# Kernel tuning notes

Hardware: AMD Instinct MI355X
Metric: run time of the kernel (lower is better)

Reference implementation:

```python
import jax, jax.numpy as jnp
import numpy as np

INPUT_DIM = 1024
EMBED_DIM = 256


def setup_inputs() -> dict:
    key = jax.random.key(0)
    ks = jax.random.split(key, 7)
    s_in = 1.0 / np.sqrt(INPUT_DIM)
    x = jax.random.normal(ks[0], (4, 2048, INPUT_DIM), dtype=jnp.float32)
    Wq = jax.random.uniform(ks[1], (INPUT_DIM, EMBED_DIM), jnp.float32, -s_in, s_in)
    bq = jax.random.uniform(ks[2], (EMBED_DIM,), jnp.float32, -s_in, s_in)
    Wk = jax.random.uniform(ks[3], (INPUT_DIM, EMBED_DIM), jnp.float32, -s_in, s_in)
    bk = jax.random.uniform(ks[4], (EMBED_DIM,), jnp.float32, -s_in, s_in)
    Wv = jax.random.uniform(ks[5], (INPUT_DIM, EMBED_DIM), jnp.float32, -s_in, s_in)
    bv = jax.random.uniform(ks[6], (EMBED_DIM,), jnp.float32, -s_in, s_in)
    return {"x": x, "Wq": Wq, "bq": bq, "Wk": Wk, "bk": bk, "Wv": Wv, "bv": bv}


def reference(x, Wq, bq, Wk, bk, Wv, bv):
    # B,T,C -> single-head attention. NOTE: original multiplies by C**0.5.
    C = x.shape[-1]
    scale = jnp.asarray(C, x.dtype) ** 0.5
    q = jnp.einsum('btc,ce->bte', x, Wq) + bq  # [B,T,E]
    k = jnp.einsum('btc,ce->bte', x, Wk) + bk
    v = jnp.einsum('btc,ce->bte', x, Wv) + bv
    wei = jnp.einsum('bqe,bke->bqk', q, k) * scale  # [B,T,T]
    wei = jax.nn.softmax(wei, axis=-1)
    # dropout p=0.0 (eval): identity
    out = jnp.einsum('bqk,bke->bqe', wei, v)  # [B,T,E]
    return out
```

## Files before the change

kernel.cpp:

```cpp
#include <hip/hip_runtime.h>
#include <math.h>

#define IDIM 1024
#define EDIM 256
#define NB 4
#define NT 2048
#define NROW 8192

typedef __attribute__((ext_vector_type(8))) short short8;
typedef __attribute__((ext_vector_type(4))) float f32x4;

#define MFMA16(A,B,C) __builtin_amdgcn_mfma_f32_16x16x32_bf16(A,B,C,0,0,0)
#define GLD16(gsrc, ldst) __builtin_amdgcn_global_load_lds( \
    (const __attribute__((address_space(1))) unsigned int*)(gsrc), \
    (__attribute__((address_space(3))) unsigned int*)(ldst), 16, 0, 0)

__device__ __forceinline__ unsigned short f2bf(float x){
    unsigned u = __builtin_bit_cast(unsigned, x);
    u += 0x7fffu + ((u >> 16) & 1u);
    return (unsigned short)(u >> 16);
}
__device__ __forceinline__ float bf2f(unsigned short h){
    unsigned u = ((unsigned)h) << 16;
    return __builtin_bit_cast(float, u);
}

__global__ __launch_bounds__(256) void split_w(
    const float* __restrict__ Wq, const float* __restrict__ Wk, const float* __restrict__ Wv,
    ushort* __restrict__ Wqh, ushort* __restrict__ Wql,
    ushort* __restrict__ Wkh, ushort* __restrict__ Wkl,
    ushort* __restrict__ Wvh)
{
    int u = blockIdx.x * 256 + threadIdx.x;
    int z   = u >> 15;
    int rem = u & 32767;
    int ko  = rem >> 8;
    int e   = rem & 255;
    const float* W = (z == 0) ? Wq : (z == 1) ? Wk : Wv;
    ushort* Oh = (z == 0) ? Wqh : (z == 1) ? Wkh : Wvh;
    ushort* Ol = (z == 0) ? Wql : Wkl;
    union { ushort us[8]; uint4 v; } hi, lo;
    #pragma unroll
    for (int j = 0; j < 8; ++j) {
        float wv = W[(size_t)(ko * 8 + j) * 256 + e];
        unsigned short h = f2bf(wv);
        hi.us[j] = h;
        lo.us[j] = f2bf(wv - bf2f(h));
    }
    *(uint4*)(Oh + (size_t)e * 1024 + ko * 8) = hi.v;
    if (z < 2) *(uint4*)(Ol + (size_t)e * 1024 + ko * 8) = lo.v;
}

__global__ __launch_bounds__(256, 3) void qkv_proj(
    const float* __restrict__ X,
    const ushort* __restrict__ Whq, const ushort* __restrict__ Wlq,
    const ushort* __restrict__ Whk, const ushort* __restrict__ Wlk,
    const ushort* __restrict__ Whv,
    const float* __restrict__ bq, const float* __restrict__ bk, const float* __restrict__ bv,
    ushort* __restrict__ Qh, ushort* __restrict__ Ql,
    ushort* __restrict__ Kh, ushort* __restrict__ Kl,
    ushort* __restrict__ Vt)
{
    __shared__ ushort Ah[259 * 8], Al[259 * 8];
    __shared__ ushort Bh[512 * 8], Bl[512 * 8];

    const int tid = threadIdx.x;
    const int lane = tid & 63, w = tid >> 6;
    const int ln = tid & 15, quad = (tid >> 4) & 3;
    const int z = blockIdx.z;
    const int n0 = blockIdx.x * 128, m0 = blockIdx.y * 64;
    const ushort* Wh = (z == 0) ? Whq : (z == 1) ? Whk : Whv;
    const ushort* Wl = (z == 0) ? Wlq : Wlk;

    f32x4 acc[4][2];
    #pragma unroll
    for (int mi = 0; mi < 4; ++mi)
        #pragma unroll
        for (int ni = 0; ni < 2; ++ni) acc[mi][ni] = (f32x4){0.f, 0.f, 0.f, 0.f};

    const int am = tid >> 2, ak8 = (tid & 3) * 8;
    const float* xp = X + (size_t)(m0 + am) * IDIM + ak8;
    const ushort* bsrc0 = Wh + (size_t)(n0 + lane) * IDIM + w * 8;
    const ushort* bsrc1 = Wh + (size_t)(n0 + 64 + lane) * IDIM + w * 8;
    const ushort* blsrc0 = Wl + (size_t)(n0 + lane) * IDIM + w * 8;
    const ushort* blsrc1 = Wl + (size_t)(n0 + 64 + lane) * IDIM + w * 8;
    ushort* bd0 = Bh + (size_t)(w * 128) * 8;
    ushort* bd1 = Bh + (size_t)(w * 128 + 64) * 8;
    ushort* bld0 = Bl + (size_t)(w * 128) * 8;
    ushort* bld1 = Bl + (size_t)(w * 128 + 64) * 8;

    for (int kk = 0; kk < IDIM; kk += 32) {
        GLD16(bsrc0 + kk, bd0);
        GLD16(bsrc1 + kk, bd1);
        if (z < 2) { GLD16(blsrc0 + kk, bld0); GLD16(blsrc1 + kk, bld1); }
        {
            float4 a0 = *(const float4*)(xp + kk);
            float4 a1 = *(const float4*)(xp + kk + 4);
            float xv[8] = {a0.x, a0.y, a0.z, a0.w, a1.x, a1.y, a1.z, a1.w};
            union { ushort us[8]; uint4 v; } hi, lo;
            #pragma unroll
            for (int j = 0; j < 8; ++j) {
                unsigned short hh = f2bf(xv[j]);
                hi.us[j] = hh;
                lo.us[j] = f2bf(xv[j] - bf2f(hh));
            }
            int unit = (tid & 3) * 65 + am;
            *(uint4*)(Ah + unit * 8) = hi.v;
            if (z < 2) *(uint4*)(Al + unit * 8) = lo.v;
        }
        __syncthreads();

        short8 ah[4], al4[4];
        #pragma unroll
        for (int mi = 0; mi < 4; ++mi) {
            int au = quad * 65 + mi * 16 + ln;
            ah[mi] = *(const short8*)(Ah + au * 8);
            if (z < 2) al4[mi] = *(const short8*)(Al + au * 8);
        }
        #pragma unroll
        for (int ni = 0; ni < 2; ++ni) {
            int bu = quad * 128 + w * 32 + ni * 16 + ln;
            short8 bh = *(const short8*)(Bh + bu * 8);
            if (z < 2) {
                short8 bl = *(const short8*)(Bl + bu * 8);
                #pragma unroll
                for (int mi = 0; mi < 4; ++mi) {
                    acc[mi][ni] = MFMA16(ah[mi], bh, acc[mi][ni]);
                    acc[mi][ni] = MFMA16(ah[mi], bl, acc[mi][ni]);
                    acc[mi][ni] = MFMA16(al4[mi], bh, acc[mi][ni]);
                }
            } else {
                #pragma unroll
                for (int mi = 0; mi < 4; ++mi)
                    acc[mi][ni] = MFMA16(ah[mi], bh, acc[mi][ni]);
            }
        }
        __syncthreads();
    }

    if (z < 2) {
        ushort* OH = (z == 0) ? Qh : Kh;
        ushort* OL = (z == 0) ? Ql : Kl;
        const float* bias = (z == 0) ? bq : bk;
        const float scale = (z == 0) ? 46.16624130844683f : 1.0f;
        #pragma unroll
        for (int ni = 0; ni < 2; ++ni) {
            int col = n0 + w * 32 + ni * 16 + ln;
            float bb = bias[col];
            #pragma unroll
            for (int mi = 0; mi < 4; ++mi)
                #pragma unroll
                for (int r = 0; r < 4; ++r) {
                    int row = m0 + mi * 16 + quad * 4 + r;
                    float v = (acc[mi][ni][r] + bb) * scale;
                    unsigned short hh = f2bf(v);
                    OH[(size_t)row * EDIM + col] = hh;
                    OL[(size_t)row * EDIM + col] = f2bf(v - bf2f(hh));
                }
        }
    } else {
        #pragma unroll
        for (int ni = 0; ni < 2; ++ni) {
            int col = n0 + w * 32 + ni * 16 + ln;
            float bb = bv[col];
            #pragma unroll
            for (int mi = 0; mi < 4; ++mi) {
                int rowb = m0 + mi * 16 + quad * 4;
                union { ushort us[4]; uint2 v; } pk;
                #pragma unroll
                for (int r = 0; r < 4; ++r) pk.us[r] = f2bf(acc[mi][ni][r] + bb);
                *(uint2*)(Vt + (size_t)col * NROW + rowb) = pk.v;
            }
        }
    }
}

__global__ __launch_bounds__(256, 2) void attn(
    const ushort* __restrict__ Qh, const ushort* __restrict__ Ql,
    const ushort* __restrict__ Kh, const ushort* __restrict__ Kl,
    const ushort* __restrict__ Vt, ushort* __restrict__ Op, float* __restrict__ mlbuf)
{
    __shared__ ushort KVbuf[4096];
    __shared__ ushort Qls[16384];
    __shared__ ushort Pall[4 * 1088];

    const int tid = threadIdx.x;
    const int lane = tid & 63;
    const int ln = tid & 15, quad = (tid >> 4) & 3, w = tid >> 6;
    ushort* Qls_w = Qls + w * 4096;
    ushort* Pw = Pall + w * 1088;

    const int id = blockIdx.x;
    const int cls = id & 15;
    const int b = cls >> 2, kvq = cls & 3;
    const int qt = id >> 4;
    const int qrow0w = b * NT + qt * 64 + w * 16;
    const int kvbase = b * NT + kvq * 512;

    short8 qh8[8];
    #pragma unroll
    for (int kc = 0; kc < 8; ++kc)
        qh8[kc] = *(const short8*)(Qh + (size_t)(qrow0w + ln) * EDIM + kc * 32 + quad * 8);
    #pragma unroll
    for (int i = 0; i < 8; ++i) {
        int u = i * 64 + lane;
        int ko = u >> 4, ln2 = u & 15;
        *(uint4*)(Qls_w + u * 8) =
            *(const uint4*)(Ql + (size_t)(qrow0w + ln2) * EDIM + ko * 8);
    }

    float m_r[4], l_r[4];
    #pragma unroll
    for (int r = 0; r < 4; ++r) { m_r[r] = -3e38f; l_r[r] = 0.f; }
    f32x4 o[16];
    #pragma unroll
    for (int ni = 0; ni < 16; ++ni) o[ni] = (f32x4){0.f, 0.f, 0.f, 0.f};

    for (int t = 0; t < 8; ++t) {
        const int kv0 = kvbase + t * 64;
        f32x4 s[4];
        #pragma unroll
        for (int ni = 0; ni < 4; ++ni) s[ni] = (f32x4){0.f, 0.f, 0.f, 0.f};

        #pragma unroll
        for (int kc = 0; kc < 8; ++kc) {
            size_t goff = (size_t)(kv0 + w * 16 + (lane & 15)) * EDIM
                          + kc * 32 + (lane >> 4) * 8;
            GLD16(Kh + goff, KVbuf + w * 512);
            GLD16(Kl + goff, KVbuf + 2048 + w * 512);
            __syncthreads();
            short8 ql8 = *(const short8*)(Qls_w + ((kc * 4 + quad) * 16 + ln) * 8);
            #pragma unroll
            for (int ni = 0; ni < 4; ++ni) {
                short8 bh = *(const short8*)(KVbuf + (ni * 64 + quad * 16 + ln) * 8);
                short8 bl = *(const short8*)(KVbuf + 2048 + (ni * 64 + quad * 16 + ln) * 8);
                s[ni] = MFMA16(qh8[kc], bh, s[ni]);
                s[ni] = MFMA16(qh8[kc], bl, s[ni]);
                s[ni] = MFMA16(ql8, bh, s[ni]);
            }
            __syncthreads();
        }

        float mt[4];
        #pragma unroll
        for (int r = 0; r < 4; ++r)
            mt[r] = fmaxf(fmaxf(s[0][r], s[1][r]), fmaxf(s[2][r], s[3][r]));
        #pragma unroll
        for (int mask = 1; mask < 16; mask <<= 1)
            #pragma unroll
            for (int r = 0; r < 4; ++r)
                mt[r] = fmaxf(mt[r], __shfl_xor(mt[r], mask));
        float alpha[4];
        #pragma unroll
        for (int r = 0; r < 4; ++r) {
            float mn = fmaxf(m_r[r], mt[r]);
            alpha[r] = exp2f(m_r[r] - mn);
            m_r[r] = mn;
        }
        float ls[4] = {0.f, 0.f, 0.f, 0.f};
        #pragma unroll
        for (int ni = 0; ni < 4; ++ni) {
            int colb = ni * 16 + ln;
            #pragma unroll
            for (int r = 0; r < 4; ++r) {
                float p = exp2f(s[ni][r] - m_r[r]);
                ls[r] += p;
                Pw[((colb >> 3) * 17 + quad * 4 + r) * 8 + (colb & 7)] = f2bf(p);
            }
        }
        #pragma unroll
        for (int mask = 1; mask < 16; mask <<= 1)
            #pragma unroll
            for (int r = 0; r < 4; ++r)
                ls[r] += __shfl_xor(ls[r], mask);
        #pragma unroll
        for (int r = 0; r < 4; ++r) l_r[r] = l_r[r] * alpha[r] + ls[r];
        #pragma unroll
        for (int ni = 0; ni < 16; ++ni)
            #pragma unroll
            for (int r = 0; r < 4; ++r) o[ni][r] *= alpha[r];

        short8 apk0 = *(const short8*)(Pw + (quad * 17 + ln) * 8);
        short8 apk1 = *(const short8*)(Pw + ((4 + quad) * 17 + ln) * 8);
        #pragma unroll
        for (int vs = 0; vs < 4; ++vs) {
            size_t gv = (size_t)(vs * 64 + w * 16 + (lane & 15)) * NROW
                        + kv0 + (lane >> 4) * 8;
            GLD16(Vt + gv, KVbuf + w * 1024);
            GLD16(Vt + gv + 32, KVbuf + w * 1024 + 512);
            __syncthreads();
            #pragma unroll
            for (int ni = 0; ni < 4; ++ni) {
                short8 v0 = *(const short8*)(KVbuf + (ni * 128 + quad * 16 + ln) * 8);
                short8 v1 = *(const short8*)(KVbuf + (ni * 128 + 64 + quad * 16 + ln) * 8);
                o[vs * 4 + ni] = MFMA16(apk0, v0, o[vs * 4 + ni]);
                o[vs * 4 + ni] = MFMA16(apk1, v1, o[vs * 4 + ni]);
            }
            __syncthreads();
        }
    }

    const int p = (b * 32 + qt) * 4 + kvq;
    if (ln == 0) {
        #pragma unroll
        for (int r = 0; r < 4; ++r) {
            int row = w * 16 + quad * 4 + r;
            *(float2*)(mlbuf + ((size_t)p * 64 + row) * 2) = make_float2(m_r[r], l_r[r]);
        }
    }
    #pragma unroll
    for (int ni = 0; ni < 16; ++ni)
        #pragma unroll
        for (int r = 0; r < 4; ++r) {
            int row = w * 16 + quad * 4 + r;
            Op[(size_t)p * 16384 + row * 256 + ni * 16 + ln] = f2bf(o[ni][r]);
        }
}

__global__ __launch_bounds__(256) void attn_merge(
    const ushort* __restrict__ Op, const float* __restrict__ mlbuf, float* __restrict__ out)
{
    const int bid = blockIdx.x, t = threadIdx.x;
    const int b = bid >> 7, qt = (bid >> 2) & 31, rg = bid & 3;
    const int row = rg * 16 + (t >> 4);
    const int e0 = (t & 15) * 16;
    const int pb = (b * 32 + qt) * 4;
    float mv[4], lv[4];
    float M = -3e38f;
    #pragma unroll
    for (int w2 = 0; w2 < 4; ++w2) {
        float2 ml = *(const float2*)(mlbuf + ((size_t)(pb + w2) * 64 + row) * 2);
        mv[w2] = ml.x; lv[w2] = ml.y;
        M = fmaxf(M, ml.x);
    }
    float sc[4], denom = 0.f;
    #pragma unroll
    for (int w2 = 0; w2 < 4; ++w2) {
        sc[w2] = exp2f(mv[w2] - M);
        denom += sc[w2] * lv[w2];
    }
    float inv = 1.0f / denom;
    #pragma unroll
    for (int w2 = 0; w2 < 4; ++w2) sc[w2] *= inv;

    float acc[16] = {};
    #pragma unroll
    for (int w2 = 0; w2 < 4; ++w2) {
        const ushort* src = Op + (size_t)(pb + w2) * 16384 + row * 256 + e0;
        #pragma unroll
        for (int c = 0; c < 2; ++c) {
            union { ushort us[8]; uint4 v; } u;
            u.v = *(const uint4*)(src + c * 8);
            #pragma unroll
            for (int j = 0; j < 8; ++j)
                acc[c * 8 + j] += sc[w2] * bf2f(u.us[j]);
        }
    }
    float* op = out + ((size_t)b * NT + qt * 64 + row) * EDIM + e0;
    #pragma unroll
    for (int g = 0; g < 4; ++g)
        *(float4*)(op + g * 4) = make_float4(acc[g*4], acc[g*4+1], acc[g*4+2], acc[g*4+3]);
}

extern "C" void kernel_launch(void* const* d_in, const int* in_sizes, int n_in,
                              void* d_out, int out_size, void* d_ws, size_t ws_size,
                              hipStream_t stream) {
    const float* x  = (const float*)d_in[0];
    const float* Wq = (const float*)d_in[1];
    const float* bq = (const float*)d_in[2];
    const float* Wk = (const float*)d_in[3];
    const float* bk = (const float*)d_in[4];
    const float* Wv = (const float*)d_in[5];
    const float* bv = (const float*)d_in[6];
    float* out = (float*)d_out;

    const size_t NE = (size_t)NB * NT * EDIM;
    ushort* Qh = (ushort*)d_ws;
    ushort* Ql = Qh + NE;
    ushort* Kh = Ql + NE;
    ushort* Kl = Kh + NE;
    ushort* Vt = Kl + NE;
    ushort* Wqh = Vt + NE;
    ushort* Wql = Wqh + 256 * 1024;
    ushort* Wkh = Wql + 256 * 1024;
    ushort* Wkl = Wkh + 256 * 1024;
    ushort* Wvh = Wkl + 256 * 1024;
    ushort* Op  = Wvh + 256 * 1024;
    float*  mlb = (float*)(Op + (size_t)512 * 16384);

    split_w<<<384, 256, 0, stream>>>(Wq, Wk, Wv, Wqh, Wql, Wkh, Wkl, Wvh);
    qkv_proj<<<dim3(2, 128, 3), 256, 0, stream>>>(x, Wqh, Wql, Wkh, Wkl, Wvh,
                                                  bq, bk, bv, Qh, Ql, Kh, Kl, Vt);
    attn<<<512, 256, 0, stream>>>(Qh, Ql, Kh, Kl, Vt, Op, mlb);
    attn_merge<<<512, 256, 0, stream>>>(Op, mlb, out);
}
```

Baseline: 209.8 us.

## Triple-buffer K/V staging in attention kernel with prefetch and vmcnt waits

Replaces the synchronous load-then-barrier K and V staging in the attention loop with a three-slot LDS ring buffer. Chunks are prefetched two stages ahead via global_load_lds and gated by explicit vmcnt waits plus s_barrier, so global loads overlap the MFMA work and the number of barriers drops. Q low halves move from LDS into registers, which frees shared memory for the larger buffers but raises register pressure. LDS use grows, which may limit the two-blocks-per-CU occupancy target.

```diff
diff --git a/kernel.cpp b/kernel.cpp
--- a/kernel.cpp
+++ b/kernel.cpp
@@ -14,6 +14,11 @@
 #define GLD16(gsrc, ldst) __builtin_amdgcn_global_load_lds( \
     (const __attribute__((address_space(1))) unsigned int*)(gsrc), \
     (__attribute__((address_space(3))) unsigned int*)(ldst), 16, 0, 0)
+
+#define WAITV4() asm volatile("s_waitcnt vmcnt(4)" ::: "memory")
+#define WAITV0() asm volatile("s_waitcnt vmcnt(0)" ::: "memory")
+#define BAR() do { asm volatile("" ::: "memory"); __builtin_amdgcn_s_barrier(); \
+                   asm volatile("" ::: "memory"); } while (0)
 
 __device__ __forceinline__ unsigned short f2bf(float x){
     unsigned u = __builtin_bit_cast(unsigned, x);
@@ -175,19 +180,37 @@
     }
 }
 
+
+__device__ __forceinline__ void stageK(const ushort* __restrict__ Kh,
+                                       const ushort* __restrict__ Kl,
+                                       ushort* buf, int kv0, int kc0, int w, int lane) {
+    size_t rowoff = (size_t)(kv0 + w * 16 + (lane & 15)) * EDIM + (lane >> 4) * 8 + kc0 * 32;
+    GLD16(Kh + rowoff,      buf + w * 512);
+    GLD16(Kh + rowoff + 32, buf + 2048 + w * 512);
+    GLD16(Kl + rowoff,      buf + 4096 + w * 512);
+    GLD16(Kl + rowoff + 32, buf + 6144 + w * 512);
+}
+
+__device__ __forceinline__ void stageV(const ushort* __restrict__ Vt,
+                                       ushort* buf, int kv0, int vs0, int w, int lane) {
+    size_t gv = (size_t)(vs0 * 64 + w * 16 + (lane & 15)) * NROW + kv0 + (lane >> 4) * 8;
+    GLD16(Vt + gv,      buf + w * 1024);
+    GLD16(Vt + gv + 32, buf + w * 1024 + 512);
+    GLD16(Vt + gv + (size_t)64 * NROW,      buf + 4096 + w * 1024);
+    GLD16(Vt + gv + (size_t)64 * NROW + 32, buf + 4096 + w * 1024 + 512);
+}
+
 __global__ __launch_bounds__(256, 2) void attn(
     const ushort* __restrict__ Qh, const ushort* __restrict__ Ql,
     const ushort* __restrict__ Kh, const ushort* __restrict__ Kl,
     const ushort* __restrict__ Vt, ushort* __restrict__ Op, float* __restrict__ mlbuf)
 {
-    __shared__ ushort KVbuf[4096];
-    __shared__ ushort Qls[16384];
+    __shared__ ushort KVbuf[3 * 8192];
     __shared__ ushort Pall[4 * 1088];
 
     const int tid = threadIdx.x;
     const int lane = tid & 63;
     const int ln = tid & 15, quad = (tid >> 4) & 3, w = tid >> 6;
-    ushort* Qls_w = Qls + w * 4096;
     ushort* Pw = Pall + w * 1088;
 
     const int id = blockIdx.x;
@@ -197,16 +220,11 @@
     const int qrow0w = b * NT + qt * 64 + w * 16;
     const int kvbase = b * NT + kvq * 512;
 
-    short8 qh8[8];
-    #pragma unroll
-    for (int kc = 0; kc < 8; ++kc)
+    short8 qh8[8], ql8[8];
+    #pragma unroll
+    for (int kc = 0; kc < 8; ++kc) {
         qh8[kc] = *(const short8*)(Qh + (size_t)(qrow0w + ln) * EDIM + kc * 32 + quad * 8);
-    #pragma unroll
-    for (int i = 0; i < 8; ++i) {
-        int u = i * 64 + lane;
-        int ko = u >> 4, ln2 = u & 15;
-        *(uint4*)(Qls_w + u * 8) =
-            *(const uint4*)(Ql + (size_t)(qrow0w + ln2) * EDIM + ko * 8);
+        ql8[kc] = *(const short8*)(Ql + (size_t)(qrow0w + ln) * EDIM + kc * 32 + quad * 8);
     }
 
     float m_r[4], l_r[4];
@@ -216,6 +234,10 @@
     #pragma unroll
     for (int ni = 0; ni < 16; ++ni) o[ni] = (f32x4){0.f, 0.f, 0.f, 0.f};
 
+    stageK(Kh, Kl, KVbuf + 0 * 8192, kvbase, 0, w, lane);
+    stageK(Kh, Kl, KVbuf + 1 * 8192, kvbase, 2, w, lane);
+
+    #pragma unroll 1
     for (int t = 0; t < 8; ++t) {
         const int kv0 = kvbase + t * 64;
         f32x4 s[4];
@@ -223,22 +245,26 @@
         for (int ni = 0; ni < 4; ++ni) s[ni] = (f32x4){0.f, 0.f, 0.f, 0.f};
 
         #pragma unroll
-        for (int kc = 0; kc < 8; ++kc) {
-            size_t goff = (size_t)(kv0 + w * 16 + (lane & 15)) * EDIM
-                          + kc * 32 + (lane >> 4) * 8;
-            GLD16(Kh + goff, KVbuf + w * 512);
-            GLD16(Kl + goff, KVbuf + 2048 + w * 512);
-            __syncthreads();
-            short8 ql8 = *(const short8*)(Qls_w + ((kc * 4 + quad) * 16 + ln) * 8);
-            #pragma unroll
-            for (int ni = 0; ni < 4; ++ni) {
-                short8 bh = *(const short8*)(KVbuf + (ni * 64 + quad * 16 + ln) * 8);
-                short8 bl = *(const short8*)(KVbuf + 2048 + (ni * 64 + quad * 16 + ln) * 8);
-                s[ni] = MFMA16(qh8[kc], bh, s[ni]);
-                s[ni] = MFMA16(qh8[kc], bl, s[ni]);
-                s[ni] = MFMA16(ql8, bh, s[ni]);
-            }
-            __syncthreads();
+        for (int j = 0; j < 4; ++j) {
+            WAITV4();
+            BAR();
+            if (j < 2)      stageK(Kh, Kl, KVbuf + ((j + 2) % 3) * 8192, kv0, 2 * (j + 2), w, lane);
+            else if (j == 2) stageV(Vt, KVbuf + 1 * 8192, kv0, 0, w, lane);
+            else             stageV(Vt, KVbuf + 2 * 8192, kv0, 2, w, lane);
+
+            const ushort* bufc = KVbuf + (j % 3) * 8192;
+            #pragma unroll
+            for (int kk = 0; kk < 2; ++kk) {
+                const int kc = j * 2 + kk;
+                #pragma unroll
+                for (int ni = 0; ni < 4; ++ni) {
+                    short8 bh = *(const short8*)(bufc + kk * 2048 + (ni * 64 + quad * 16 + ln) * 8);
+                    short8 bl = *(const short8*)(bufc + 4096 + kk * 2048 + (ni * 64 + quad * 16 + ln) * 8);
+                    s[ni] = MFMA16(qh8[kc], bh, s[ni]);
+                    s[ni] = MFMA16(qh8[kc], bl, s[ni]);
+                    s[ni] = MFMA16(ql8[kc], bh, s[ni]);
+                }
+            }
         }
 
         float mt[4];
@@ -282,21 +308,27 @@
 
         short8 apk0 = *(const short8*)(Pw + (quad * 17 + ln) * 8);
         short8 apk1 = *(const short8*)(Pw + ((4 + quad) * 17 + ln) * 8);
-        #pragma unroll
-        for (int vs = 0; vs < 4; ++vs) {
-            size_t gv = (size_t)(vs * 64 + w * 16 + (lane & 15)) * NROW
-                        + kv0 + (lane >> 4) * 8;
-            GLD16(Vt + gv, KVbuf + w * 1024);
-            GLD16(Vt + gv + 32, KVbuf + w * 1024 + 512);
-            __syncthreads();
-            #pragma unroll
-            for (int ni = 0; ni < 4; ++ni) {
-                short8 v0 = *(const short8*)(KVbuf + (ni * 128 + quad * 16 + ln) * 8);
-                short8 v1 = *(const short8*)(KVbuf + (ni * 128 + 64 + quad * 16 + ln) * 8);
-                o[vs * 4 + ni] = MFMA16(apk0, v0, o[vs * 4 + ni]);
-                o[vs * 4 + ni] = MFMA16(apk1, v1, o[vs * 4 + ni]);
-            }
-            __syncthreads();
+
+        #pragma unroll
+        for (int j2 = 0; j2 < 2; ++j2) {
+            if (t < 7 || j2 == 0) { WAITV4(); } else { WAITV0(); }
+            BAR();
+            if (t < 7) {
+                if (j2 == 0) stageK(Kh, Kl, KVbuf + 0 * 8192, kv0 + 64, 0, w, lane);
+                else         stageK(Kh, Kl, KVbuf + 1 * 8192, kv0 + 64, 2, w, lane);
+            }
+            const ushort* bufc = KVbuf + (1 + j2) * 8192;
+            #pragma unroll
+            for (int vv = 0; vv < 2; ++vv) {
+                const int vs = j2 * 2 + vv;
+                #pragma unroll
+                for (int ni = 0; ni < 4; ++ni) {
+                    short8 v0 = *(const short8*)(bufc + vv * 4096 + (ni * 128 + quad * 16 + ln) * 8);
+                    short8 v1 = *(const short8*)(bufc + vv * 4096 + (ni * 128 + 64 + quad * 16 + ln) * 8);
+                    o[vs * 4 + ni] = MFMA16(apk0, v0, o[vs * 4 + ni]);
+                    o[vs * 4 + ni] = MFMA16(apk1, v1, o[vs * 4 + ni]);
+                }
+            }
         }
     }
 
```

Result: no change. 206.1 us (-1.7%).
